# Kernel optimization log

Hardware: AMD Instinct MI355X
Metric: run time of the kernel (lower is better)

Reference implementation:

```python
import jax, jax.numpy as jnp
import numpy as np


def setup_inputs() -> dict:
    key = jax.random.key(0)
    kx, kw, kb = jax.random.split(key, 3)
    B, D, L, W = 2, 4096, 4096, 4
    # int8 quantized input / weight / bias (stored as int8, full [-128,127] range)
    x = jax.random.randint(kx, (B, D, L), -128, 128, dtype=jnp.int32).astype(jnp.int8)
    weight = jax.random.randint(kw, (D, W), -128, 128, dtype=jnp.int32).astype(jnp.int8)
    bias = jax.random.randint(kb, (D,), -128, 128, dtype=jnp.int32).astype(jnp.int8)
    return {
        "x": x,
        "weight": weight,
        "bias": bias,
        "input_scale": jnp.float32(0.05),
        "weight_scale": jnp.float32(0.002),
        "output_scale": jnp.float32(0.05),
        "bias_scale": jnp.float32(0.01),
    }


def _causal_dw_conv(xf, wf):
    # xf: [B, D, L] float, wf: [D, W] float; depthwise causal conv (left pad W-1)
    D, W = wf.shape
    return jax.lax.conv_general_dilated(
        xf, wf[:, None, :],  # [D, 1, W] OIH with feature_group_count=D -> depthwise
        window_strides=(1,), padding=[(W - 1, 0)],
        dimension_numbers=("NCH", "OIH", "NCH"), feature_group_count=D)


def reference(x, weight, bias, input_scale, weight_scale, output_scale, bias_scale):
    # fused dequant -> causal depthwise conv -> bias -> SiLU -> requant to int8
    xf = x.astype(jnp.float32) * input_scale
    wf = weight.astype(jnp.float32) * weight_scale
    bf = bias.astype(jnp.float32) * bias_scale
    y = _causal_dw_conv(xf, wf) + bf[None, :, None]
    y = jax.nn.silu(y)  # causal_conv1d activation=True -> SiLU
    q = jnp.clip(jnp.round(y / output_scale), -128.0, 127.0).astype(jnp.int8)
    return q
```

## Files before the change

kernel.cpp:

```cpp
#include <hip/hip_runtime.h>


#define DMASK 4095
#define CPR   1024
#define CPRM  1023
#define CSHIFT 10
#define NCHUNKS 8388608
#define STRIDE  524288
#define ITERS   16

typedef int iv4 __attribute__((ext_vector_type(4)));

__device__ __forceinline__ int silu_requant(float y, float inv_out) {
    float e = __expf(-y);
    float s = y * __builtin_amdgcn_rcpf(1.0f + e);
    float q = rintf(s * inv_out);
    q = fminf(fmaxf(q, -128.0f), 127.0f);
    return (int)q;
}

__global__ __launch_bounds__(256) void qconv1d_kernel(
    const int* __restrict__ x,
    const int* __restrict__ w,
    const int* __restrict__ bias,
    const float* __restrict__ in_s_p,
    const float* __restrict__ w_s_p,
    const float* __restrict__ out_s_p,
    const float* __restrict__ b_s_p,
    int* __restrict__ out)
{
    const int base = blockIdx.x * 256 + threadIdx.x;

    const float s_xw    = in_s_p[0] * w_s_p[0];
    const float inv_out = 1.0f / out_s_p[0];
    const float b_s     = b_s_p[0];

    const iv4* __restrict__ xv = (const iv4*)x;
    iv4* __restrict__ ov = (iv4*)out;

    #pragma unroll 4
    for (int it = 0; it < ITERS; ++it) {
        const int chunk = base + it * STRIDE;
        const int d     = (chunk >> CSHIFT) & DMASK;
        const bool interior = (chunk & CPRM) != 0;

        const int hchunk = (chunk == 0) ? 0 : chunk - 1;
        iv4 cur = xv[chunk];
        iv4 hal = xv[hchunk];

        int py = interior ? hal.y : 0;
        int pz = interior ? hal.z : 0;
        int pw = interior ? hal.w : 0;

        const int du = __builtin_amdgcn_readfirstlane(d);
        iv4 wv = ((const iv4*)w)[du];
        const float bf = (float)bias[du] * b_s;

        float w0 = (float)wv.x, w1 = (float)wv.y, w2 = (float)wv.z, w3 = (float)wv.w;
        float p1 = (float)py, p2 = (float)pz, p3 = (float)pw;
        float c0 = (float)cur.x, c1 = (float)cur.y, c2 = (float)cur.z, c3 = (float)cur.w;

        float a0 = w0*p1 + w1*p2 + w2*p3 + w3*c0;
        float a1 = w0*p2 + w1*p3 + w2*c0 + w3*c1;
        float a2 = w0*p3 + w1*c0 + w2*c1 + w3*c2;
        float a3 = w0*c0 + w1*c1 + w2*c2 + w3*c3;

        float y0 = a0 * s_xw + bf;
        float y1 = a1 * s_xw + bf;
        float y2 = a2 * s_xw + bf;
        float y3 = a3 * s_xw + bf;

        iv4 q;
        q.x = silu_requant(y0, inv_out);
        q.y = silu_requant(y1, inv_out);
        q.z = silu_requant(y2, inv_out);
        q.w = silu_requant(y3, inv_out);

        ov[chunk] = q;
    }
}

extern "C" void kernel_launch(void* const* d_in, const int* in_sizes, int n_in,
                              void* d_out, int out_size, void* d_ws, size_t ws_size,
                              hipStream_t stream) {
    const int*   x    = (const int*)d_in[0];
    const int*   w    = (const int*)d_in[1];
    const int*   bias = (const int*)d_in[2];
    const float* is   = (const float*)d_in[3];
    const float* ws   = (const float*)d_in[4];
    const float* os   = (const float*)d_in[5];
    const float* bs   = (const float*)d_in[6];
    int* out = (int*)d_out;

    qconv1d_kernel<<<2048, 256, 0, stream>>>(x, w, bias, is, ws, os, bs, out);
}
```

Before: 242.6 us.

## Assign one row per wavefront, share halo via lane shuffles, prefetch next chunks

Each wavefront now handles a whole (batch, channel) row of the sequence instead of strided chunks scattered across rows. The three-element causal halo is passed between lanes and between iterations with __shfl_up and __shfl, so the second global load per chunk goes away. Weight and bias are loaded once per wave instead of once per iteration. Each iteration issues the loads for the next pair of chunks before computing the current pair. This removes redundant memory traffic and per-iteration address work, at the cost of extra cross-lane shuffles and higher register pressure.

```diff
diff --git a/kernel.cpp b/kernel.cpp
--- a/kernel.cpp
+++ b/kernel.cpp
@@ -2,13 +2,6 @@
 
 
 #define DMASK 4095
-#define CPR   1024
-#define CPRM  1023
-#define CSHIFT 10
-#define NCHUNKS 8388608
-#define STRIDE  524288
-#define ITERS   16
-
 typedef int iv4 __attribute__((ext_vector_type(4)));
 
 __device__ __forceinline__ int silu_requant(float y, float inv_out) {
@@ -17,6 +10,23 @@
     float q = rintf(s * inv_out);
     q = fminf(fmaxf(q, -128.0f), 127.0f);
     return (int)q;
+}
+
+__device__ __forceinline__ iv4 conv_chunk(iv4 c, int p1, int p2, int p3,
+                                          float w0, float w1, float w2, float w3,
+                                          float s_xw, float bf, float inv_out) {
+    float f1 = (float)p1, f2 = (float)p2, f3 = (float)p3;
+    float c0 = (float)c.x, c1 = (float)c.y, c2 = (float)c.z, c3 = (float)c.w;
+    float a0 = w0*f1 + w1*f2 + w2*f3 + w3*c0;
+    float a1 = w0*f2 + w1*f3 + w2*c0 + w3*c1;
+    float a2 = w0*f3 + w1*c0 + w2*c1 + w3*c2;
+    float a3 = w0*c0 + w1*c1 + w2*c2 + w3*c3;
+    iv4 q;
+    q.x = silu_requant(a0 * s_xw + bf, inv_out);
+    q.y = silu_requant(a1 * s_xw + bf, inv_out);
+    q.z = silu_requant(a2 * s_xw + bf, inv_out);
+    q.w = silu_requant(a3 * s_xw + bf, inv_out);
+    return q;
 }
 
 __global__ __launch_bounds__(256) void qconv1d_kernel(
@@ -29,54 +39,53 @@
     const float* __restrict__ b_s_p,
     int* __restrict__ out)
 {
-    const int base = blockIdx.x * 256 + threadIdx.x;
+    const int lane = threadIdx.x & 63;
+    const int row  = blockIdx.x * 4 + (threadIdx.x >> 6);
+    const int d    = row & DMASK;
 
     const float s_xw    = in_s_p[0] * w_s_p[0];
     const float inv_out = 1.0f / out_s_p[0];
-    const float b_s     = b_s_p[0];
+
+    const int du = __builtin_amdgcn_readfirstlane(d);
+    iv4 wv = ((const iv4*)w)[du];
+    const float bf = (float)bias[du] * b_s_p[0];
+    const float w0 = (float)wv.x, w1 = (float)wv.y,
+                w2 = (float)wv.z, w3 = (float)wv.w;
 
     const iv4* __restrict__ xv = (const iv4*)x;
     iv4* __restrict__ ov = (iv4*)out;
+    const int cbase = row << 10;
 
-    #pragma unroll 4
-    for (int it = 0; it < ITERS; ++it) {
-        const int chunk = base + it * STRIDE;
-        const int d     = (chunk >> CSHIFT) & DMASK;
-        const bool interior = (chunk & CPRM) != 0;
+    iv4 A = xv[cbase + lane];
+    iv4 B = xv[cbase + 64 + lane];
 
-        const int hchunk = (chunk == 0) ? 0 : chunk - 1;
-        iv4 cur = xv[chunk];
-        iv4 hal = xv[hchunk];
+    int cy = 0, cz = 0, cw = 0;
+    const bool l0 = (lane == 0);
 
-        int py = interior ? hal.y : 0;
-        int pz = interior ? hal.z : 0;
-        int pw = interior ? hal.w : 0;
+    #pragma unroll
+    for (int it = 0; it < 8; ++it) {
+        iv4 An, Bn;
+        if (it < 7) {
+            An = xv[cbase + (it + 1) * 128 + lane];
+            Bn = xv[cbase + (it + 1) * 128 + 64 + lane];
+        }
 
-        const int du = __builtin_amdgcn_readfirstlane(d);
-        iv4 wv = ((const iv4*)w)[du];
-        const float bf = (float)bias[du] * b_s;
+        int ay = __shfl_up(A.y, 1), az = __shfl_up(A.z, 1), aw = __shfl_up(A.w, 1);
+        ay = l0 ? cy : ay;  az = l0 ? cz : az;  aw = l0 ? cw : aw;
 
-        float w0 = (float)wv.x, w1 = (float)wv.y, w2 = (float)wv.z, w3 = (float)wv.w;
-        float p1 = (float)py, p2 = (float)pz, p3 = (float)pw;
-        float c0 = (float)cur.x, c1 = (float)cur.y, c2 = (float)cur.z, c3 = (float)cur.w;
+        int by = __shfl_up(B.y, 1), bz = __shfl_up(B.z, 1), bw = __shfl_up(B.w, 1);
+        int a63y = __shfl(A.y, 63), a63z = __shfl(A.z, 63), a63w = __shfl(A.w, 63);
+        by = l0 ? a63y : by;  bz = l0 ? a63z : bz;  bw = l0 ? a63w : bw;
 
-        float a0 = w0*p1 + w1*p2 + w2*p3 + w3*c0;
-        float a1 = w0*p2 + w1*p3 + w2*c0 + w3*c1;
-        float a2 = w0*p3 + w1*c0 + w2*c1 + w3*c2;
-        float a3 = w0*c0 + w1*c1 + w2*c2 + w3*c3;
+        cy = __shfl(B.y, 63);  cz = __shfl(B.z, 63);  cw = __shfl(B.w, 63);
 
-        float y0 = a0 * s_xw + bf;
-        float y1 = a1 * s_xw + bf;
-        float y2 = a2 * s_xw + bf;
-        float y3 = a3 * s_xw + bf;
+        iv4 qA = conv_chunk(A, ay, az, aw, w0, w1, w2, w3, s_xw, bf, inv_out);
+        iv4 qB = conv_chunk(B, by, bz, bw, w0, w1, w2, w3, s_xw, bf, inv_out);
 
-        iv4 q;
-        q.x = silu_requant(y0, inv_out);
-        q.y = silu_requant(y1, inv_out);
-        q.z = silu_requant(y2, inv_out);
-        q.w = silu_requant(y3, inv_out);
+        ov[cbase + it * 128 + lane]      = qA;
+        ov[cbase + it * 128 + 64 + lane] = qB;
 
-        ov[chunk] = q;
+        A = An;  B = Bn;
     }
 }
 
```

Result: no change. 246.1 us (+1.4%).
